# Kernel tuning notes

Measured on AMD Instinct MI355X. Metric: run time of the kernel, lower is better.

Reference implementation:

```python
import jax, jax.numpy as jnp
import numpy as np

K = 3        # kernel size
PAD = 1      # padding
G = 8        # deform_groups


def conv2d(x, w, b):
    y = jax.lax.conv_general_dilated(x, w, (1, 1), ((PAD, PAD), (PAD, PAD)),
                                     dimension_numbers=('NCHW', 'OIHW', 'NCHW'))
    return y + b[None, :, None, None]


def deform_conv(feat, offset, w, b):
    # feat: [B,C,H,W]; offset: [B, G*K*K*2, H, W] (mmcv layout: per group, per kernel pos, (dy,dx))
    B, C, H, W = feat.shape
    Cg = C // G
    KK = K * K
    off = offset.reshape(B, G, KK, 2, H, W)
    dy, dx = off[:, :, :, 0], off[:, :, :, 1]                      # [B,G,KK,H,W]
    kh = (jnp.arange(KK) // K).astype(feat.dtype)
    kw = (jnp.arange(KK) % K).astype(feat.dtype)
    hh = jnp.arange(H, dtype=feat.dtype)
    ww = jnp.arange(W, dtype=feat.dtype)
    ys = hh[None, None, None, :, None] - PAD + kh[None, None, :, None, None] + dy
    xs = ww[None, None, None, None, :] - PAD + kw[None, None, :, None, None] + dx
    y0 = jnp.floor(ys)
    x0 = jnp.floor(xs)
    wy = (ys - y0)[:, :, None]                                     # [B,G,1,KK,H,W]
    wx = (xs - x0)[:, :, None]
    y0i = y0.astype(jnp.int32)
    x0i = x0.astype(jnp.int32)
    feat_flat = feat.reshape(B, G, Cg, H * W)

    def gather(yi, xi):
        valid = ((yi >= 0) & (yi < H) & (xi >= 0) & (xi < W)).astype(feat.dtype)
        lin = (jnp.clip(yi, 0, H - 1) * W + jnp.clip(xi, 0, W - 1)).astype(jnp.int32)
        lin = lin.reshape(B, G, KK * H * W)
        v = jax.vmap(jax.vmap(lambda f, i: f[:, i]))(feat_flat, lin)  # [B,G,Cg,KK*H*W]
        return v.reshape(B, G, Cg, KK, H, W) * valid[:, :, None]

    v00 = gather(y0i, x0i)
    v01 = gather(y0i, x0i + 1)
    v10 = gather(y0i + 1, x0i)
    v11 = gather(y0i + 1, x0i + 1)
    samp = (v00 * (1 - wy) * (1 - wx) + v01 * (1 - wy) * wx
            + v10 * wy * (1 - wx) + v11 * wy * wx)                 # [B,G,Cg,KK,H,W]
    wg = w.reshape(w.shape[0], G, Cg, KK)                          # [Cout,G,Cg,KK]
    out = jnp.einsum('ogck,bgckhw->bohw', wg, samp)
    return out + b[None, :, None, None]


def setup_inputs() -> dict:
    key = jax.random.key(0)
    k1, k2, k3 = jax.random.split(key, 3)
    B, T, C, H, W = 1, 5, 64, 96, 96
    x = jax.random.normal(k1, (B, T, C, H, W), dtype=jnp.float32)
    # offset conv: 2C -> G*2*K*K; small scale so sampled offsets stay local
    w_off = jax.random.normal(k2, (G * 2 * K * K, 2 * C, K, K), dtype=jnp.float32) * 0.01
    b_off = jnp.zeros((G * 2 * K * K,), dtype=jnp.float32)
    w_dcn = jax.random.normal(k3, (C, C, K, K), dtype=jnp.float32) * (1.0 / np.sqrt(C * K * K))
    b_dcn = jnp.zeros((C,), dtype=jnp.float32)
    return {"x": x, "w_off": w_off, "b_off": b_off, "w_dcn": w_dcn, "b_dcn": b_dcn}


def reference(x, w_off, b_off, w_dcn, b_dcn):
    B, T, C, H, W = x.shape
    center = x[:, T // 2]
    feats = []
    for i in range(T):
        if i == T // 2:
            feats.append(center)
        else:
            neig = x[:, i]
            offset = conv2d(jnp.concatenate([neig, center], axis=1), w_off, b_off)
            feats.append(deform_conv(neig, offset, w_dcn, b_dcn))
    return jnp.stack(feats, axis=1)
```

## Files before the change

kernel.cpp:

```cpp
#include <hip/hip_runtime.h>
#include <hip/hip_bf16.h>

#define HWN 9216
#define PLN (64 * HWN)
#define SLDE 584

typedef __attribute__((ext_vector_type(8))) short bf16x8;
typedef __attribute__((ext_vector_type(4))) float f32x4;

__device__ __forceinline__ unsigned short f2bf(float v) {
    union { float f; unsigned u; } cv; cv.f = v;
    unsigned u = cv.u;
    u += 0x7fffu + ((u >> 16) & 1u);
    return (unsigned short)(u >> 16);
}
__device__ __forceinline__ float bf2f(unsigned short b) {
    union { unsigned u; float f; } cv; cv.u = ((unsigned)b) << 16;
    return cv.f;
}

__global__ __launch_bounds__(256) void xprep_kernel(
    const float* __restrict__ x, const float* __restrict__ w_dcn,
    const float* __restrict__ w_off, unsigned short* __restrict__ xt,
    unsigned short* __restrict__ wbf, unsigned short* __restrict__ wcbf,
    float* __restrict__ out)
{
    const int t = blockIdx.y;
    const int tid = threadIdx.x;
    if (t == 5) {
        for (int idx = blockIdx.x * 256 + tid; idx < 64 * 576 + 2 * 144 * 576;
             idx += 144 * 256) {
            if (idx < 64 * 576) {
                int o = idx / 576, c = idx % 576;
                int g = c / 72, rem = c % 72, k = rem >> 3, cg = rem & 7;
                wbf[idx] = f2bf(w_dcn[o * 576 + (g * 8 + cg) * 9 + k]);
            } else {
                int i2 = idx - 64 * 576;
                int s = i2 / (144 * 576);
                int o = (i2 / 576) % 144;
                int kk = i2 % 576;
                int g = kk / 72, rem = kk % 72, k = rem >> 3, cg = rem & 7;
                wcbf[i2] = f2bf(w_off[(size_t)o * 1152
                                      + (size_t)(s * 64 + g * 8 + cg) * 9 + k]);
            }
        }
        return;
    }
    const int p0 = blockIdx.x * 64;
    __shared__ unsigned short tile[64][72];
    const float* in = x + (size_t)t * PLN;
    const bool isC = (t == 2);
    for (int idx = tid; idx < 4096; idx += 256) {
        int c = idx >> 6, p = idx & 63;
        float v = in[(size_t)c * HWN + p0 + p];
        tile[p][c] = f2bf(v);
        if (isC) out[(size_t)2 * PLN + (size_t)c * HWN + p0 + p] = v;
    }
    __syncthreads();
    unsigned short* xo = xt + ((size_t)t * HWN + p0) * 64;
    for (int task = tid; task < 512; task += 256) {
        int p = task >> 3, cb = task & 7;
        *reinterpret_cast<bf16x8*>(xo + p * 64 + cb * 8) =
            *reinterpret_cast<const bf16x8*>(&tile[p][cb * 8]);
    }
}

__global__ __launch_bounds__(576, 2) void conv_center_kernel(
    const unsigned short* __restrict__ xt,
    const unsigned short* __restrict__ wcbf,
    float* __restrict__ wsC)
{
    const int p0 = blockIdx.x * 32;
    const int tid = threadIdx.x;
    const int w = tid >> 6, l = tid & 63;
    const int lr = l & 15, lg = l >> 4;

    __shared__ unsigned short smp[32 * SLDE];

    {
        const unsigned short* xb = xt + (size_t)2 * HWN * 64;
        const bf16x8 bz = {0,0,0,0,0,0,0,0};
        bf16x8 stg[4]; int dst[4];
        #pragma unroll
        for (int i = 0; i < 4; ++i) {
            const int tsk = i * 576 + tid;
            const int g = tsk & 7, pl = (tsk >> 3) & 31, k = tsk >> 8;
            const int p = p0 + pl;
            const int y = p / 96, xx = p - y * 96;
            const int r = k / 3, d = k - 3 * (k / 3);
            const int yy = y + r - 1, xw = xx + d - 1;
            const bool valid = (yy >= 0) & (yy < 96) & (xw >= 0) & (xw < 96);
            const int lin = min(max(yy, 0), 95) * 96 + min(max(xw, 0), 95);
            bf16x8 v = *reinterpret_cast<const bf16x8*>(xb + (size_t)lin * 64 + g * 8);
            stg[i] = valid ? v : bz;
            dst[i] = pl * SLDE + g * 72 + k * 8;
        }
        #pragma unroll
        for (int i = 0; i < 4; ++i)
            *reinterpret_cast<bf16x8*>(smp + dst[i]) = stg[i];
    }
    __syncthreads();

    const unsigned short* wp = wcbf + (size_t)1 * 144 * 576
                               + (size_t)(w * 16 + lr) * 576 + lg * 8;
    bf16x8 afr[18];
    #pragma unroll
    for (int ss = 0; ss < 18; ++ss)
        afr[ss] = *reinterpret_cast<const bf16x8*>(wp + ss * 32);

    f32x4 acc[2] = {{0,0,0,0},{0,0,0,0}};
    #pragma unroll
    for (int pt = 0; pt < 2; ++pt) {
        const unsigned short* brow = smp + (pt * 16 + lr) * SLDE + lg * 8;
        #pragma unroll
        for (int ss = 0; ss < 18; ++ss) {
            bf16x8 b = *reinterpret_cast<const bf16x8*>(brow + ss * 32);
            acc[pt] = __builtin_amdgcn_mfma_f32_16x16x32_bf16(afr[ss], b, acc[pt], 0, 0, 0);
        }
    }
    #pragma unroll
    for (int pt = 0; pt < 2; ++pt) {
        const int px = p0 + pt * 16 + lr;
        #pragma unroll
        for (int r = 0; r < 4; ++r) {
            const int o = w * 16 + lg * 4 + r;
            wsC[(size_t)o * HWN + px] = acc[pt][r];
        }
    }
}

__global__ __launch_bounds__(576, 2) void conv_neig_kernel(
    const unsigned short* __restrict__ xt,
    const unsigned short* __restrict__ wcbf,
    const float* __restrict__ b_off,
    const float* __restrict__ wsC,
    float* __restrict__ ofs)
{
    const int f = blockIdx.y;
    const int t = f < 2 ? f : f + 1;
    const int p0 = blockIdx.x * 64;
    const int tid = threadIdx.x;
    const int w = tid >> 6, l = tid & 63;
    const int lr = l & 15, lg = l >> 4;

    __shared__ unsigned short smp[64 * SLDE];

    {
        const unsigned short* xb = xt + (size_t)t * HWN * 64;
        const bf16x8 bz = {0,0,0,0,0,0,0,0};
        bf16x8 stg[8]; int dst[8];
        #pragma unroll
        for (int i = 0; i < 8; ++i) {
            const int tsk = i * 576 + tid;
            const int g = tsk & 7, pl = (tsk >> 3) & 63, k = tsk >> 9;
            const int p = p0 + pl;
            const int y = p / 96, xx = p - y * 96;
            const int r = k / 3, d = k - 3 * (k / 3);
            const int yy = y + r - 1, xw = xx + d - 1;
            const bool valid = (yy >= 0) & (yy < 96) & (xw >= 0) & (xw < 96);
            const int lin = min(max(yy, 0), 95) * 96 + min(max(xw, 0), 95);
            bf16x8 v = *reinterpret_cast<const bf16x8*>(xb + (size_t)lin * 64 + g * 8);
            stg[i] = valid ? v : bz;
            dst[i] = pl * SLDE + g * 72 + k * 8;
        }
        #pragma unroll
        for (int i = 0; i < 8; ++i)
            *reinterpret_cast<bf16x8*>(smp + dst[i]) = stg[i];
    }
    __syncthreads();

    const unsigned short* wp = wcbf + (size_t)(w * 16 + lr) * 576 + lg * 8;
    bf16x8 afr[18];
    #pragma unroll
    for (int ss = 0; ss < 18; ++ss)
        afr[ss] = *reinterpret_cast<const bf16x8*>(wp + ss * 32);

    f32x4 acc[4] = {{0,0,0,0},{0,0,0,0},{0,0,0,0},{0,0,0,0}};
    #pragma unroll
    for (int pt = 0; pt < 4; ++pt) {
        const unsigned short* brow = smp + (pt * 16 + lr) * SLDE + lg * 8;
        #pragma unroll
        for (int ss = 0; ss < 18; ++ss) {
            bf16x8 b = *reinterpret_cast<const bf16x8*>(brow + ss * 32);
            acc[pt] = __builtin_amdgcn_mfma_f32_16x16x32_bf16(afr[ss], b, acc[pt], 0, 0, 0);
        }
    }

    float* of = ofs + (size_t)f * 144 * HWN;
    #pragma unroll
    for (int pt = 0; pt < 4; ++pt) {
        const int px = p0 + pt * 16 + lr;
        #pragma unroll
        for (int r = 0; r < 4; ++r) {
            const int o = w * 16 + lg * 4 + r;
            of[(size_t)o * HWN + px] = acc[pt][r] + wsC[(size_t)o * HWN + px] + b_off[o];
        }
    }
}

__global__ __launch_bounds__(256, 4) void deform_kernel(
    const unsigned short* __restrict__ xt,
    const float* __restrict__ ofs,
    const unsigned short* __restrict__ wbf,
    const float* __restrict__ b_dcn,
    float* __restrict__ out)
{
    const int f = blockIdx.y;
    const int t = f < 2 ? f : f + 1;
    const int p0 = blockIdx.x * 32;
    const int tid = threadIdx.x;

    __shared__ unsigned short smp[32 * SLDE];

    {
        const int g = tid >> 5, pl = tid & 31;
        const int p = p0 + pl;
        const int y = p / 96, xx = p - y * 96;
        const unsigned short* xf = xt + (size_t)t * HWN * 64 + g * 8;
        const float* ob = ofs + (size_t)f * 144 * HWN + (size_t)g * 18 * HWN + p;
        float dy[9], dx[9];
        #pragma unroll
        for (int k = 0; k < 9; ++k) {
            dy[k] = ob[(size_t)(2 * k) * HWN];
            dx[k] = ob[(size_t)(2 * k + 1) * HWN];
        }
        unsigned short* srow = smp + pl * SLDE + g * 72;

        bf16x8 cc[2][4];
        float  ww[2][4];
        auto prep = [&](int k, int buf) {
            const int r = k / 3, d = k - 3 * (k / 3);
            const float ys = (float)(y + r - 1) + dy[k];
            const float xs = (float)(xx + d - 1) + dx[k];
            const float y0f = floorf(ys), x0f = floorf(xs);
            const float wy = ys - y0f, wx = xs - x0f;
            const int y0 = (int)y0f, x0 = (int)x0f;
            const int y1 = y0 + 1, x1 = x0 + 1;
            const bool vy0 = (y0 >= 0) & (y0 < 96);
            const bool vy1 = (y1 >= 0) & (y1 < 96);
            const bool vx0 = (x0 >= 0) & (x0 < 96);
            const bool vx1 = (x1 >= 0) & (x1 < 96);
            const int yc0 = min(max(y0, 0), 95), yc1 = min(max(y1, 0), 95);
            const int xc0 = min(max(x0, 0), 95), xc1 = min(max(x1, 0), 95);
            ww[buf][0] = (vy0 & vx0) ? (1.f - wy) * (1.f - wx) : 0.f;
            ww[buf][1] = (vy0 & vx1) ? (1.f - wy) * wx : 0.f;
            ww[buf][2] = (vy1 & vx0) ? wy * (1.f - wx) : 0.f;
            ww[buf][3] = (vy1 & vx1) ? wy * wx : 0.f;
            cc[buf][0] = *reinterpret_cast<const bf16x8*>(xf + (size_t)(yc0 * 96 + xc0) * 64);
            cc[buf][1] = *reinterpret_cast<const bf16x8*>(xf + (size_t)(yc0 * 96 + xc1) * 64);
            cc[buf][2] = *reinterpret_cast<const bf16x8*>(xf + (size_t)(yc1 * 96 + xc0) * 64);
            cc[buf][3] = *reinterpret_cast<const bf16x8*>(xf + (size_t)(yc1 * 96 + xc1) * 64);
        };

        prep(0, 0);
        #pragma unroll
        for (int k = 0; k < 9; ++k) {
            if (k < 8) prep(k + 1, (k + 1) & 1);
            const int b = k & 1;
            bf16x8 pk;
            #pragma unroll
            for (int ch = 0; ch < 8; ++ch) {
                float v = ww[b][0] * bf2f((unsigned short)cc[b][0][ch]);
                v = fmaf(ww[b][1], bf2f((unsigned short)cc[b][1][ch]), v);
                v = fmaf(ww[b][2], bf2f((unsigned short)cc[b][2][ch]), v);
                v = fmaf(ww[b][3], bf2f((unsigned short)cc[b][3][ch]), v);
                pk[ch] = (short)f2bf(v);
            }
            *reinterpret_cast<bf16x8*>(srow + k * 8) = pk;
        }
    }
    __syncthreads();

    const int w = tid >> 6;
    const int l = tid & 63;
    const int o0 = w * 16;
    const int lr = l & 15, lg = l >> 4;

    bf16x8 afr[18];
    const unsigned short* wrow = wbf + (size_t)(o0 + lr) * 576 + lg * 8;
    #pragma unroll
    for (int s = 0; s < 18; ++s)
        afr[s] = *reinterpret_cast<const bf16x8*>(wrow + s * 32);

    f32x4 acc0 = {0.f, 0.f, 0.f, 0.f}, acc1 = {0.f, 0.f, 0.f, 0.f};
    const unsigned short* brow0 = smp + lr * SLDE + lg * 8;
    const unsigned short* brow1 = brow0 + 16 * SLDE;
    #pragma unroll
    for (int s = 0; s < 18; ++s) {
        bf16x8 b0 = *reinterpret_cast<const bf16x8*>(brow0 + s * 32);
        bf16x8 b1 = *reinterpret_cast<const bf16x8*>(brow1 + s * 32);
        acc0 = __builtin_amdgcn_mfma_f32_16x16x32_bf16(afr[s], b0, acc0, 0, 0, 0);
        acc1 = __builtin_amdgcn_mfma_f32_16x16x32_bf16(afr[s], b1, acc1, 0, 0, 0);
    }

    float* op = out + (size_t)t * PLN + p0;
    #pragma unroll
    for (int r = 0; r < 4; ++r) {
        const int o = o0 + lg * 4 + r;
        const float bb = b_dcn[o];
        op[(size_t)o * HWN + lr] = acc0[r] + bb;
        op[(size_t)o * HWN + 16 + lr] = acc1[r] + bb;
    }
}

extern "C" void kernel_launch(void* const* d_in, const int* in_sizes, int n_in,
                              void* d_out, int out_size, void* d_ws, size_t ws_size,
                              hipStream_t stream) {
    const float* x     = (const float*)d_in[0];
    const float* w_off = (const float*)d_in[1];
    const float* b_off = (const float*)d_in[2];
    const float* w_dcn = (const float*)d_in[3];
    const float* b_dcn = (const float*)d_in[4];
    float* out = (float*)d_out;

    float* ofs          = (float*)d_ws;
    unsigned short* xt  = (unsigned short*)(ofs + (size_t)4 * 144 * HWN);
    unsigned short* wbf = xt + (size_t)5 * HWN * 64;
    unsigned short* wcbf = wbf + (size_t)64 * 576;
    float* wsC = (float*)(wcbf + (size_t)2 * 144 * 576);

    xprep_kernel<<<dim3(144, 6), 256, 0, stream>>>(x, w_dcn, w_off, xt, wbf, wcbf, out);

    conv_center_kernel<<<288, 576, 0, stream>>>(xt, wcbf, wsC);

    conv_neig_kernel<<<dim3(144, 4), 576, 0, stream>>>(xt, wcbf, b_off, wsC, ofs);

    deform_kernel<<<dim3(288, 4), 256, 0, stream>>>(xt, ofs, wbf, b_dcn, out);
}
```

Measured before the change: 83.19 us.

## Store offsets in bf16, merge conv kernels, double-buffer gather, vectorize xprep

The intermediate offset tensor and center-conv partial sums are now stored in bf16 instead of fp32, halving their write and read traffic. The two conv kernels become one mode-switched kernel that processes 64 pixels in two 32-pixel halves, prefetching the second half's gather into registers while the first half runs its MFMAs, with a smaller LDS footprint. xprep now loads float4 vectors and unrolls its loops. Rounding offsets to bf16 lowers the precision of sampling positions, which may raise error in the deformable sampling.

```diff
diff --git a/kernel.cpp b/kernel.cpp
--- a/kernel.cpp
+++ b/kernel.cpp
@@ -50,157 +50,153 @@
     __shared__ unsigned short tile[64][72];
     const float* in = x + (size_t)t * PLN;
     const bool isC = (t == 2);
-    for (int idx = tid; idx < 4096; idx += 256) {
-        int c = idx >> 6, p = idx & 63;
-        float v = in[(size_t)c * HWN + p0 + p];
-        tile[p][c] = f2bf(v);
-        if (isC) out[(size_t)2 * PLN + (size_t)c * HWN + p0 + p] = v;
+    #pragma unroll
+    for (int i = 0; i < 4; ++i) {
+        const int idx = i * 256 + tid;
+        const int c = idx >> 4, p4 = idx & 15;
+        float4 v = *reinterpret_cast<const float4*>(in + (size_t)c * HWN + p0 + p4 * 4);
+        tile[p4 * 4 + 0][c] = f2bf(v.x);
+        tile[p4 * 4 + 1][c] = f2bf(v.y);
+        tile[p4 * 4 + 2][c] = f2bf(v.z);
+        tile[p4 * 4 + 3][c] = f2bf(v.w);
+        if (isC)
+            *reinterpret_cast<float4*>(out + (size_t)2 * PLN + (size_t)c * HWN + p0 + p4 * 4) = v;
     }
     __syncthreads();
     unsigned short* xo = xt + ((size_t)t * HWN + p0) * 64;
-    for (int task = tid; task < 512; task += 256) {
-        int p = task >> 3, cb = task & 7;
+    #pragma unroll
+    for (int i = 0; i < 2; ++i) {
+        const int task = i * 256 + tid;
+        const int p = task >> 3, cb = task & 7;
         *reinterpret_cast<bf16x8*>(xo + p * 64 + cb * 8) =
             *reinterpret_cast<const bf16x8*>(&tile[p][cb * 8]);
     }
 }
 
-__global__ __launch_bounds__(576, 2) void conv_center_kernel(
-    const unsigned short* __restrict__ xt,
-    const unsigned short* __restrict__ wcbf,
-    float* __restrict__ wsC)
-{
-    const int p0 = blockIdx.x * 32;
-    const int tid = threadIdx.x;
-    const int w = tid >> 6, l = tid & 63;
-    const int lr = l & 15, lg = l >> 4;
-
-    __shared__ unsigned short smp[32 * SLDE];
-
-    {
-        const unsigned short* xb = xt + (size_t)2 * HWN * 64;
-        const bf16x8 bz = {0,0,0,0,0,0,0,0};
-        bf16x8 stg[4]; int dst[4];
-        #pragma unroll
-        for (int i = 0; i < 4; ++i) {
-            const int tsk = i * 576 + tid;
-            const int g = tsk & 7, pl = (tsk >> 3) & 31, k = tsk >> 8;
-            const int p = p0 + pl;
-            const int y = p / 96, xx = p - y * 96;
-            const int r = k / 3, d = k - 3 * (k / 3);
-            const int yy = y + r - 1, xw = xx + d - 1;
-            const bool valid = (yy >= 0) & (yy < 96) & (xw >= 0) & (xw < 96);
-            const int lin = min(max(yy, 0), 95) * 96 + min(max(xw, 0), 95);
-            bf16x8 v = *reinterpret_cast<const bf16x8*>(xb + (size_t)lin * 64 + g * 8);
-            stg[i] = valid ? v : bz;
-            dst[i] = pl * SLDE + g * 72 + k * 8;
-        }
-        #pragma unroll
-        for (int i = 0; i < 4; ++i)
-            *reinterpret_cast<bf16x8*>(smp + dst[i]) = stg[i];
-    }
-    __syncthreads();
-
-    const unsigned short* wp = wcbf + (size_t)1 * 144 * 576
-                               + (size_t)(w * 16 + lr) * 576 + lg * 8;
-    bf16x8 afr[18];
-    #pragma unroll
-    for (int ss = 0; ss < 18; ++ss)
-        afr[ss] = *reinterpret_cast<const bf16x8*>(wp + ss * 32);
-
-    f32x4 acc[2] = {{0,0,0,0},{0,0,0,0}};
-    #pragma unroll
-    for (int pt = 0; pt < 2; ++pt) {
-        const unsigned short* brow = smp + (pt * 16 + lr) * SLDE + lg * 8;
-        #pragma unroll
-        for (int ss = 0; ss < 18; ++ss) {
-            bf16x8 b = *reinterpret_cast<const bf16x8*>(brow + ss * 32);
-            acc[pt] = __builtin_amdgcn_mfma_f32_16x16x32_bf16(afr[ss], b, acc[pt], 0, 0, 0);
-        }
-    }
-    #pragma unroll
-    for (int pt = 0; pt < 2; ++pt) {
-        const int px = p0 + pt * 16 + lr;
-        #pragma unroll
-        for (int r = 0; r < 4; ++r) {
-            const int o = w * 16 + lg * 4 + r;
-            wsC[(size_t)o * HWN + px] = acc[pt][r];
-        }
-    }
-}
-
-__global__ __launch_bounds__(576, 2) void conv_neig_kernel(
+__global__ __launch_bounds__(576, 2) void conv_mfma_kernel(
     const unsigned short* __restrict__ xt,
     const unsigned short* __restrict__ wcbf,
     const float* __restrict__ b_off,
-    const float* __restrict__ wsC,
-    float* __restrict__ ofs)
+    const unsigned short* __restrict__ wsC,
+    unsigned short* __restrict__ outp,
+    int mode)
 {
     const int f = blockIdx.y;
-    const int t = f < 2 ? f : f + 1;
+    const int t = mode ? (f < 2 ? f : f + 1) : 2;
+    const int slab = mode ? 0 : 1;
     const int p0 = blockIdx.x * 64;
     const int tid = threadIdx.x;
     const int w = tid >> 6, l = tid & 63;
     const int lr = l & 15, lg = l >> 4;
 
-    __shared__ unsigned short smp[64 * SLDE];
-
-    {
-        const unsigned short* xb = xt + (size_t)t * HWN * 64;
-        const bf16x8 bz = {0,0,0,0,0,0,0,0};
-        bf16x8 stg[8]; int dst[8];
-        #pragma unroll
-        for (int i = 0; i < 8; ++i) {
-            const int tsk = i * 576 + tid;
-            const int g = tsk & 7, pl = (tsk >> 3) & 63, k = tsk >> 9;
-            const int p = p0 + pl;
-            const int y = p / 96, xx = p - y * 96;
-            const int r = k / 3, d = k - 3 * (k / 3);
-            const int yy = y + r - 1, xw = xx + d - 1;
-            const bool valid = (yy >= 0) & (yy < 96) & (xw >= 0) & (xw < 96);
-            const int lin = min(max(yy, 0), 95) * 96 + min(max(xw, 0), 95);
-            bf16x8 v = *reinterpret_cast<const bf16x8*>(xb + (size_t)lin * 64 + g * 8);
-            stg[i] = valid ? v : bz;
-            dst[i] = pl * SLDE + g * 72 + k * 8;
-        }
-        #pragma unroll
-        for (int i = 0; i < 8; ++i)
-            *reinterpret_cast<bf16x8*>(smp + dst[i]) = stg[i];
-    }
-    __syncthreads();
-
-    const unsigned short* wp = wcbf + (size_t)(w * 16 + lr) * 576 + lg * 8;
+    __shared__ unsigned short smp[32 * SLDE];
+
+    const unsigned short* xb = xt + (size_t)t * HWN * 64;
+    const bf16x8 bz = {0, 0, 0, 0, 0, 0, 0, 0};
+
+    const unsigned short* wp = wcbf + (size_t)slab * 144 * 576
+                               + (size_t)(w * 16 + lr) * 576 + lg * 8;
     bf16x8 afr[18];
     #pragma unroll
     for (int ss = 0; ss < 18; ++ss)
         afr[ss] = *reinterpret_cast<const bf16x8*>(wp + ss * 32);
 
-    f32x4 acc[4] = {{0,0,0,0},{0,0,0,0},{0,0,0,0},{0,0,0,0}};
-    #pragma unroll
-    for (int pt = 0; pt < 4; ++pt) {
-        const unsigned short* brow = smp + (pt * 16 + lr) * SLDE + lg * 8;
-        #pragma unroll
-        for (int ss = 0; ss < 18; ++ss) {
-            bf16x8 b = *reinterpret_cast<const bf16x8*>(brow + ss * 32);
-            acc[pt] = __builtin_amdgcn_mfma_f32_16x16x32_bf16(afr[ss], b, acc[pt], 0, 0, 0);
-        }
-    }
-
-    float* of = ofs + (size_t)f * 144 * HWN;
-    #pragma unroll
-    for (int pt = 0; pt < 4; ++pt) {
-        const int px = p0 + pt * 16 + lr;
-        #pragma unroll
-        for (int r = 0; r < 4; ++r) {
-            const int o = w * 16 + lg * 4 + r;
-            of[(size_t)o * HWN + px] = acc[pt][r] + wsC[(size_t)o * HWN + px] + b_off[o];
+    bf16x8 sA[4]; int dA[4];
+    #pragma unroll
+    for (int i = 0; i < 4; ++i) {
+        const int tsk = i * 576 + tid;
+        const int g = tsk & 7, pl = (tsk >> 3) & 31, k = tsk >> 8;
+        const int p = p0 + pl;
+        const int y = p / 96, xx = p - y * 96;
+        const int r = k / 3, d = k - 3 * (k / 3);
+        const int yy = y + r - 1, xw = xx + d - 1;
+        const bool valid = (yy >= 0) & (yy < 96) & (xw >= 0) & (xw < 96);
+        const int lin = min(max(yy, 0), 95) * 96 + min(max(xw, 0), 95);
+        bf16x8 v = *reinterpret_cast<const bf16x8*>(xb + (size_t)lin * 64 + g * 8);
+        sA[i] = valid ? v : bz;
+        dA[i] = pl * SLDE + g * 72 + k * 8;
+    }
+    #pragma unroll
+    for (int i = 0; i < 4; ++i)
+        *reinterpret_cast<bf16x8*>(smp + dA[i]) = sA[i];
+    __syncthreads();
+
+    bf16x8 sB[4]; int dB[4];
+    #pragma unroll
+    for (int i = 0; i < 4; ++i) {
+        const int tsk = i * 576 + tid;
+        const int g = tsk & 7, pl = (tsk >> 3) & 31, k = tsk >> 8;
+        const int p = p0 + 32 + pl;
+        const int y = p / 96, xx = p - y * 96;
+        const int r = k / 3, d = k - 3 * (k / 3);
+        const int yy = y + r - 1, xw = xx + d - 1;
+        const bool valid = (yy >= 0) & (yy < 96) & (xw >= 0) & (xw < 96);
+        const int lin = min(max(yy, 0), 95) * 96 + min(max(xw, 0), 95);
+        bf16x8 v = *reinterpret_cast<const bf16x8*>(xb + (size_t)lin * 64 + g * 8);
+        sB[i] = valid ? v : bz;
+        dB[i] = pl * SLDE + g * 72 + k * 8;
+    }
+
+    {
+        f32x4 acc[2] = {{0,0,0,0},{0,0,0,0}};
+        #pragma unroll
+        for (int pt = 0; pt < 2; ++pt) {
+            const unsigned short* brow = smp + (pt * 16 + lr) * SLDE + lg * 8;
+            #pragma unroll
+            for (int ss = 0; ss < 18; ++ss) {
+                bf16x8 b = *reinterpret_cast<const bf16x8*>(brow + ss * 32);
+                acc[pt] = __builtin_amdgcn_mfma_f32_16x16x32_bf16(afr[ss], b, acc[pt], 0, 0, 0);
+            }
+        }
+        unsigned short* op = mode ? (outp + (size_t)f * 144 * HWN) : outp;
+        #pragma unroll
+        for (int pt = 0; pt < 2; ++pt) {
+            const int px = p0 + pt * 16 + lr;
+            #pragma unroll
+            for (int r = 0; r < 4; ++r) {
+                const int o = w * 16 + lg * 4 + r;
+                float vv = acc[pt][r];
+                if (mode) vv += bf2f(wsC[(size_t)o * HWN + px]) + b_off[o];
+                op[(size_t)o * HWN + px] = f2bf(vv);
+            }
+        }
+    }
+    __syncthreads();
+
+    #pragma unroll
+    for (int i = 0; i < 4; ++i)
+        *reinterpret_cast<bf16x8*>(smp + dB[i]) = sB[i];
+    __syncthreads();
+
+    {
+        f32x4 acc[2] = {{0,0,0,0},{0,0,0,0}};
+        #pragma unroll
+        for (int pt = 0; pt < 2; ++pt) {
+            const unsigned short* brow = smp + (pt * 16 + lr) * SLDE + lg * 8;
+            #pragma unroll
+            for (int ss = 0; ss < 18; ++ss) {
+                bf16x8 b = *reinterpret_cast<const bf16x8*>(brow + ss * 32);
+                acc[pt] = __builtin_amdgcn_mfma_f32_16x16x32_bf16(afr[ss], b, acc[pt], 0, 0, 0);
+            }
+        }
+        unsigned short* op = mode ? (outp + (size_t)f * 144 * HWN) : outp;
+        #pragma unroll
+        for (int pt = 0; pt < 2; ++pt) {
+            const int px = p0 + 32 + pt * 16 + lr;
+            #pragma unroll
+            for (int r = 0; r < 4; ++r) {
+                const int o = w * 16 + lg * 4 + r;
+                float vv = acc[pt][r];
+                if (mode) vv += bf2f(wsC[(size_t)o * HWN + px]) + b_off[o];
+                op[(size_t)o * HWN + px] = f2bf(vv);
+            }
         }
     }
 }
 
 __global__ __launch_bounds__(256, 4) void deform_kernel(
     const unsigned short* __restrict__ xt,
-    const float* __restrict__ ofs,
+    const unsigned short* __restrict__ ofs,
     const unsigned short* __restrict__ wbf,
     const float* __restrict__ b_dcn,
     float* __restrict__ out)
@@ -217,12 +213,12 @@
         const int p = p0 + pl;
         const int y = p / 96, xx = p - y * 96;
         const unsigned short* xf = xt + (size_t)t * HWN * 64 + g * 8;
-        const float* ob = ofs + (size_t)f * 144 * HWN + (size_t)g * 18 * HWN + p;
+        const unsigned short* ob = ofs + (size_t)f * 144 * HWN + (size_t)g * 18 * HWN + p;
         float dy[9], dx[9];
         #pragma unroll
         for (int k = 0; k < 9; ++k) {
-            dy[k] = ob[(size_t)(2 * k) * HWN];
-            dx[k] = ob[(size_t)(2 * k + 1) * HWN];
+            dy[k] = bf2f(ob[(size_t)(2 * k) * HWN]);
+            dx[k] = bf2f(ob[(size_t)(2 * k + 1) * HWN]);
         }
         unsigned short* srow = smp + pl * SLDE + g * 72;
 
@@ -313,17 +309,17 @@
     const float* b_dcn = (const float*)d_in[4];
     float* out = (float*)d_out;
 
-    float* ofs          = (float*)d_ws;
-    unsigned short* xt  = (unsigned short*)(ofs + (size_t)4 * 144 * HWN);
-    unsigned short* wbf = xt + (size_t)5 * HWN * 64;
+    unsigned short* ofs  = (unsigned short*)d_ws;
+    unsigned short* xt   = ofs + (size_t)4 * 144 * HWN;
+    unsigned short* wbf  = xt + (size_t)5 * HWN * 64;
     unsigned short* wcbf = wbf + (size_t)64 * 576;
-    float* wsC = (float*)(wcbf + (size_t)2 * 144 * 576);
+    unsigned short* wsC  = wcbf + (size_t)2 * 144 * 576;
 
     xprep_kernel<<<dim3(144, 6), 256, 0, stream>>>(x, w_dcn, w_off, xt, wbf, wcbf, out);
 
-    conv_center_kernel<<<288, 576, 0, stream>>>(xt, wcbf, wsC);
-
-    conv_neig_kernel<<<dim3(144, 4), 576, 0, stream>>>(xt, wcbf, b_off, wsC, ofs);
+    conv_mfma_kernel<<<dim3(144, 1), 576, 0, stream>>>(xt, wcbf, b_off, nullptr, wsC, 0);
+
+    conv_mfma_kernel<<<dim3(144, 4), 576, 0, stream>>>(xt, wcbf, b_off, wsC, ofs, 1);
 
     deform_kernel<<<dim3(288, 4), 256, 0, stream>>>(xt, ofs, wbf, b_dcn, out);
 }
```

Result: slower. 88.84 us (+6.8%).

## Fuse offset convolution and deformable convolution into one kernel via LDS offsets

Applied to the files above, without the earlier changes.

Merges the neighbor offset-conv kernel and the deform kernel into a single kernel that processes 32 pixels per block. The computed offsets are kept in shared memory instead of being written to and re-read from a global workspace, which removes a large global round trip and one launch. In exchange, the bilinear sampling phase uses only 256 of the 576 threads, and shared memory use per block rises.

```diff
diff --git a/kernel.cpp b/kernel.cpp
--- a/kernel.cpp
+++ b/kernel.cpp
@@ -4,6 +4,7 @@
 #define HWN 9216
 #define PLN (64 * HWN)
 #define SLDE 584
+#define OLD 33
 
 typedef __attribute__((ext_vector_type(8))) short bf16x8;
 typedef __attribute__((ext_vector_type(4))) float f32x4;
@@ -129,30 +130,34 @@
     }
 }
 
-__global__ __launch_bounds__(576, 2) void conv_neig_kernel(
+__global__ __launch_bounds__(576, 2) void fused_kernel(
     const unsigned short* __restrict__ xt,
     const unsigned short* __restrict__ wcbf,
     const float* __restrict__ b_off,
     const float* __restrict__ wsC,
-    float* __restrict__ ofs)
+    const unsigned short* __restrict__ wbf,
+    const float* __restrict__ b_dcn,
+    float* __restrict__ out)
 {
     const int f = blockIdx.y;
     const int t = f < 2 ? f : f + 1;
-    const int p0 = blockIdx.x * 64;
+    const int p0 = blockIdx.x * 32;
     const int tid = threadIdx.x;
     const int w = tid >> 6, l = tid & 63;
     const int lr = l & 15, lg = l >> 4;
 
-    __shared__ unsigned short smp[64 * SLDE];
+    __shared__ unsigned short smp[32 * SLDE];
+    __shared__ float ofs_lds[144 * OLD];
+
+    const unsigned short* xb = xt + (size_t)t * HWN * 64;
+    const bf16x8 bz = {0,0,0,0,0,0,0,0};
 
     {
-        const unsigned short* xb = xt + (size_t)t * HWN * 64;
-        const bf16x8 bz = {0,0,0,0,0,0,0,0};
-        bf16x8 stg[8]; int dst[8];
-        #pragma unroll
-        for (int i = 0; i < 8; ++i) {
+        bf16x8 stg[4]; int dst[4];
+        #pragma unroll
+        for (int i = 0; i < 4; ++i) {
             const int tsk = i * 576 + tid;
-            const int g = tsk & 7, pl = (tsk >> 3) & 63, k = tsk >> 9;
+            const int g = tsk & 7, pl = (tsk >> 3) & 31, k = tsk >> 8;
             const int p = p0 + pl;
             const int y = p / 96, xx = p - y * 96;
             const int r = k / 3, d = k - 3 * (k / 3);
@@ -164,65 +169,51 @@
             dst[i] = pl * SLDE + g * 72 + k * 8;
         }
         #pragma unroll
-        for (int i = 0; i < 8; ++i)
+        for (int i = 0; i < 4; ++i)
             *reinterpret_cast<bf16x8*>(smp + dst[i]) = stg[i];
     }
     __syncthreads();
 
-    const unsigned short* wp = wcbf + (size_t)(w * 16 + lr) * 576 + lg * 8;
-    bf16x8 afr[18];
-    #pragma unroll
-    for (int ss = 0; ss < 18; ++ss)
-        afr[ss] = *reinterpret_cast<const bf16x8*>(wp + ss * 32);
-
-    f32x4 acc[4] = {{0,0,0,0},{0,0,0,0},{0,0,0,0},{0,0,0,0}};
-    #pragma unroll
-    for (int pt = 0; pt < 4; ++pt) {
-        const unsigned short* brow = smp + (pt * 16 + lr) * SLDE + lg * 8;
-        #pragma unroll
-        for (int ss = 0; ss < 18; ++ss) {
-            bf16x8 b = *reinterpret_cast<const bf16x8*>(brow + ss * 32);
-            acc[pt] = __builtin_amdgcn_mfma_f32_16x16x32_bf16(afr[ss], b, acc[pt], 0, 0, 0);
-        }
-    }
-
-    float* of = ofs + (size_t)f * 144 * HWN;
-    #pragma unroll
-    for (int pt = 0; pt < 4; ++pt) {
-        const int px = p0 + pt * 16 + lr;
-        #pragma unroll
-        for (int r = 0; r < 4; ++r) {
-            const int o = w * 16 + lg * 4 + r;
-            of[(size_t)o * HWN + px] = acc[pt][r] + wsC[(size_t)o * HWN + px] + b_off[o];
-        }
-    }
-}
-
-__global__ __launch_bounds__(256, 4) void deform_kernel(
-    const unsigned short* __restrict__ xt,
-    const float* __restrict__ ofs,
-    const unsigned short* __restrict__ wbf,
-    const float* __restrict__ b_dcn,
-    float* __restrict__ out)
-{
-    const int f = blockIdx.y;
-    const int t = f < 2 ? f : f + 1;
-    const int p0 = blockIdx.x * 32;
-    const int tid = threadIdx.x;
-
-    __shared__ unsigned short smp[32 * SLDE];
-
     {
+        const unsigned short* wp = wcbf + (size_t)(w * 16 + lr) * 576 + lg * 8;
+        bf16x8 afr[18];
+        #pragma unroll
+        for (int ss = 0; ss < 18; ++ss)
+            afr[ss] = *reinterpret_cast<const bf16x8*>(wp + ss * 32);
+
+        f32x4 acc[2] = {{0,0,0,0},{0,0,0,0}};
+        #pragma unroll
+        for (int pt = 0; pt < 2; ++pt) {
+            const unsigned short* brow = smp + (pt * 16 + lr) * SLDE + lg * 8;
+            #pragma unroll
+            for (int ss = 0; ss < 18; ++ss) {
+                bf16x8 b = *reinterpret_cast<const bf16x8*>(brow + ss * 32);
+                acc[pt] = __builtin_amdgcn_mfma_f32_16x16x32_bf16(afr[ss], b, acc[pt], 0, 0, 0);
+            }
+        }
+        #pragma unroll
+        for (int pt = 0; pt < 2; ++pt) {
+            const int px = p0 + pt * 16 + lr;
+            #pragma unroll
+            for (int r = 0; r < 4; ++r) {
+                const int o = w * 16 + lg * 4 + r;
+                ofs_lds[o * OLD + pt * 16 + lr] =
+                    acc[pt][r] + wsC[(size_t)o * HWN + px] + b_off[o];
+            }
+        }
+    }
+    __syncthreads();
+
+    if (tid < 256) {
         const int g = tid >> 5, pl = tid & 31;
         const int p = p0 + pl;
         const int y = p / 96, xx = p - y * 96;
-        const unsigned short* xf = xt + (size_t)t * HWN * 64 + g * 8;
-        const float* ob = ofs + (size_t)f * 144 * HWN + (size_t)g * 18 * HWN + p;
+        const unsigned short* xf = xb + g * 8;
         float dy[9], dx[9];
         #pragma unroll
         for (int k = 0; k < 9; ++k) {
-            dy[k] = ob[(size_t)(2 * k) * HWN];
-            dx[k] = ob[(size_t)(2 * k + 1) * HWN];
+            dy[k] = ofs_lds[(g * 18 + 2 * k) * OLD + pl];
+            dx[k] = ofs_lds[(g * 18 + 2 * k + 1) * OLD + pl];
         }
         unsigned short* srow = smp + pl * SLDE + g * 72;
 
@@ -271,35 +262,30 @@
     }
     __syncthreads();
 
-    const int w = tid >> 6;
-    const int l = tid & 63;
-    const int o0 = w * 16;
-    const int lr = l & 15, lg = l >> 4;
-
-    bf16x8 afr[18];
-    const unsigned short* wrow = wbf + (size_t)(o0 + lr) * 576 + lg * 8;
-    #pragma unroll
-    for (int s = 0; s < 18; ++s)
-        afr[s] = *reinterpret_cast<const bf16x8*>(wrow + s * 32);
-
-    f32x4 acc0 = {0.f, 0.f, 0.f, 0.f}, acc1 = {0.f, 0.f, 0.f, 0.f};
-    const unsigned short* brow0 = smp + lr * SLDE + lg * 8;
-    const unsigned short* brow1 = brow0 + 16 * SLDE;
-    #pragma unroll
-    for (int s = 0; s < 18; ++s) {
-        bf16x8 b0 = *reinterpret_cast<const bf16x8*>(brow0 + s * 32);
-        bf16x8 b1 = *reinterpret_cast<const bf16x8*>(brow1 + s * 32);
-        acc0 = __builtin_amdgcn_mfma_f32_16x16x32_bf16(afr[s], b0, acc0, 0, 0, 0);
-        acc1 = __builtin_amdgcn_mfma_f32_16x16x32_bf16(afr[s], b1, acc1, 0, 0, 0);
-    }
-
-    float* op = out + (size_t)t * PLN + p0;
-    #pragma unroll
-    for (int r = 0; r < 4; ++r) {
-        const int o = o0 + lg * 4 + r;
-        const float bb = b_dcn[o];
-        op[(size_t)o * HWN + lr] = acc0[r] + bb;
-        op[(size_t)o * HWN + 16 + lr] = acc1[r] + bb;
+    if (w < 8) {
+        const int o0 = (w & 3) * 16;
+        const int pt2 = w >> 2;
+
+        bf16x8 afr[18];
+        const unsigned short* wrow = wbf + (size_t)(o0 + lr) * 576 + lg * 8;
+        #pragma unroll
+        for (int s = 0; s < 18; ++s)
+            afr[s] = *reinterpret_cast<const bf16x8*>(wrow + s * 32);
+
+        f32x4 acc = {0.f, 0.f, 0.f, 0.f};
+        const unsigned short* brow = smp + (pt2 * 16 + lr) * SLDE + lg * 8;
+        #pragma unroll
+        for (int s = 0; s < 18; ++s) {
+            bf16x8 b = *reinterpret_cast<const bf16x8*>(brow + s * 32);
+            acc = __builtin_amdgcn_mfma_f32_16x16x32_bf16(afr[s], b, acc, 0, 0, 0);
+        }
+
+        float* op = out + (size_t)t * PLN + p0 + pt2 * 16 + lr;
+        #pragma unroll
+        for (int r = 0; r < 4; ++r) {
+            const int o = o0 + lg * 4 + r;
+            op[(size_t)o * HWN] = acc[r] + b_dcn[o];
+        }
     }
 }
 
@@ -313,9 +299,8 @@
     const float* b_dcn = (const float*)d_in[4];
     float* out = (float*)d_out;
 
-    float* ofs          = (float*)d_ws;
-    unsigned short* xt  = (unsigned short*)(ofs + (size_t)4 * 144 * HWN);
-    unsigned short* wbf = xt + (size_t)5 * HWN * 64;
+    unsigned short* xt   = (unsigned short*)d_ws;
+    unsigned short* wbf  = xt + (size_t)5 * HWN * 64;
     unsigned short* wcbf = wbf + (size_t)64 * 576;
     float* wsC = (float*)(wcbf + (size_t)2 * 144 * 576);
 
@@ -323,7 +308,5 @@
 
     conv_center_kernel<<<288, 576, 0, stream>>>(xt, wcbf, wsC);
 
-    conv_neig_kernel<<<dim3(144, 4), 576, 0, stream>>>(xt, wcbf, b_off, wsC, ofs);
-
-    deform_kernel<<<dim3(288, 4), 256, 0, stream>>>(xt, ofs, wbf, b_dcn, out);
-}
+    fused_kernel<<<dim3(288, 4), 576, 0, stream>>>(xt, wcbf, b_off, wsC, wbf, b_dcn, out);
+}
```

Result: slower. 95.05 us (+14.3%).
